# Performance work log

Measured on AMD Instinct MI355X. Metric: run time of the kernel, lower is better.

The kernel has to match this reference:

```python
import jax, jax.numpy as jnp
import numpy as np

B, N, M = 4, 50000, 256
BIN_MIN, BIN_MAX = -3.0, 3.0


def setup_inputs() -> dict:
    key = jax.random.key(0)
    kx, ky = jax.random.split(key)
    x_coords = jax.random.normal(kx, (B, N), dtype=jnp.float32)
    y_coords = jax.random.normal(ky, (B, N), dtype=jnp.float32)
    bins = jnp.linspace(BIN_MIN, BIN_MAX, M, dtype=jnp.float32)
    return {"x_coords": x_coords, "y_coords": y_coords, "bins": bins}


def reference(x_coords, y_coords, bins):
    # bandwidth defaults to bin resolution (bins[1] - bins[0])
    bandwidth = bins[1] - bins[0]
    # per-axis Gaussian kernel values: (B, N, M)
    kx = jnp.exp(-0.5 * jnp.square((x_coords[..., None] - bins) / bandwidth))
    ky = jnp.exp(-0.5 * jnp.square((y_coords[..., None] - bins) / bandwidth))
    # joint kernel values reduced over particles: (B, M, M)
    joint = jnp.einsum("bni,bnj->bij", kx, ky)
    norm = jnp.sum(joint, axis=(-2, -1), keepdims=True) + 1e-10
    return joint / norm
```

## Files before the change

### kernel.cpp

```cpp
#include <hip/hip_runtime.h>


#define B_     4
#define N_     50000
#define M_     256
#define NCH    32
#define NST    2
#define CHUNK  ((N_ + NCH - 1) / NCH)
#define BLOCK  1024
#define NWAVE  (BLOCK / 64)
#define GROWS  128
#define GCELLS (GROWS * M_)
#define GP64   16384
#define G64SZ  16576
#define CS2    0.72134752f
#define L127   6.9886847f

#if __has_builtin(__builtin_amdgcn_exp2f)
  #define EXP2(t) __builtin_amdgcn_exp2f(t)
#else
  #define EXP2(t) exp2f(t)
#endif

__device__ __forceinline__ unsigned short bf16ru(float f) {
    return (unsigned short)((__builtin_bit_cast(unsigned, f) + 0x8000u) >> 16);
}
__device__ __forceinline__ float bf2f(unsigned short u) {
    return __builtin_bit_cast(float, ((unsigned)u) << 16);
}

__global__ __launch_bounds__(BLOCK) void kde_accum(
    const float* __restrict__ xs, const float* __restrict__ ys,
    const float* __restrict__ bins, unsigned short* __restrict__ partial,
    float* __restrict__ ws2, int wide)
{
    __shared__ __align__(16) unsigned long long G64[G64SZ];
    __shared__ float sred[NWAVE];

    const int tid   = threadIdx.x;
    const int strip = blockIdx.x;
    const int chunk = blockIdx.y;
    const int b     = blockIdx.z;
    const int lane  = tid & 63;
    const int w     = tid >> 6;

    const float bin0  = bins[0];
    const float invbw = 1.0f / (bins[1] - bin0);
    const int   rlo   = strip * GROWS;

    {
        uint4* gz = (uint4*)G64;
        const uint4 z4 = {0u, 0u, 0u, 0u};
        for (int t = tid; t < G64SZ / 2; t += BLOCK) gz[t] = z4;
    }
    __syncthreads();

    const int start = chunk * CHUNK;
    const int end   = (start + CHUNK < N_) ? (start + CHUNK) : N_;
    const float* xp = xs + (size_t)b * N_;
    const float* yp = ys + (size_t)b * N_;

    const unsigned dmp = (unsigned)(GP64 + lane);

    int k = start + tid;
    float x = 3.0e30f, y = 3.0e30f;
    if (k < end) { x = xp[k]; y = yp[k]; }
    for (; k < end; k += BLOCK) {
        float xn = 3.0e30f, yn = 3.0e30f;
        if (k + BLOCK < end) { xn = xp[k + BLOCK]; yn = yp[k + BLOCK]; }

        const float ux  = (x - bin0) * invbw;
        const float uy  = (y - bin0) * invbw;
        const float stx = rintf(ux) - 3.0f;
        const float sty = rintf(uy) - 3.0f;
        const int rx = (int)stx;
        const int ry = (int)sty;

        if (rx + 6 >= rlo && rx < rlo + GROWS && ry + 6 >= 0 && ry < M_) {
            const float dx0 = ux - stx;
            const float dy0 = uy - sty;
            unsigned qx[7], qy[7];
            #pragma unroll
            for (int j = 0; j < 7; ++j) {
                const float dx = dx0 - (float)j;
                const float dy = dy0 - (float)j;
                qx[j] = (unsigned)(int)(EXP2(fmaf(-CS2 * dx, dx, L127)) + 0.5f);
                qy[j] = (unsigned)(int)(EXP2(fmaf(-CS2 * dy, dy, L127)) + 0.5f);
            }
            const int s  = ry & 1;
            const int pb0 = (ry - s) >> 1;
            const unsigned lo0 = s ? 0u    : qy[0], hi0 = s ? qy[0] : qy[1];
            const unsigned lo1 = s ? qy[1] : qy[2], hi1 = s ? qy[2] : qy[3];
            const unsigned lo2 = s ? qy[3] : qy[4], hi2 = s ? qy[4] : qy[5];
            const unsigned lo3 = s ? qy[5] : qy[6], hi3 = s ? qy[6] : 0u;
            unsigned long long ypk[4];
            ypk[0] = (unsigned long long)lo0 | ((unsigned long long)hi0 << 32);
            ypk[1] = (unsigned long long)lo1 | ((unsigned long long)hi1 << 32);
            ypk[2] = (unsigned long long)lo2 | ((unsigned long long)hi2 << 32);
            ypk[3] = (unsigned long long)lo3 | ((unsigned long long)hi3 << 32);
            unsigned pofs[4];
            #pragma unroll
            for (int t = 0; t < 4; ++t) {
                const int p = pb0 + t;
                pofs[t] = ((unsigned)p < 128u) ? (unsigned)p : 0x80000000u;
            }
            #pragma unroll
            for (int i = 0; i < 7; ++i) {
                const int rr = rx + i - rlo;
                const unsigned rbase =
                    ((unsigned)rr < (unsigned)GROWS) ? (unsigned)(rr << 7) : dmp;
                const unsigned long long wxi = (unsigned long long)qx[i];
                #pragma unroll
                for (int t = 0; t < 4; ++t) {
                    unsigned a = rbase + pofs[t];
                    a = ((int)a < 0) ? dmp : a;
                    atomicAdd(&G64[a], wxi * ypk[t]);
                }
            }
        }
        x = xn; y = yn;
    }
    __syncthreads();

    const unsigned int* Gv = (const unsigned int*)G64;
    unsigned short* pb = partial + (((size_t)chunk * B_ + b) << 16);
    float tsum = 0.f;
    #pragma unroll
    for (int rep = 0; rep < GCELLS / (BLOCK * 4); ++rep) {
        const int cell = rep * (BLOCK * 4) + tid * 4;
        const uint4 gv = *(const uint4*)&Gv[cell];
        const float f0 = (float)gv.x, f1 = (float)gv.y;
        const float f2 = (float)gv.z, f3 = (float)gv.w;
        tsum += (f0 + f1) + (f2 + f3);
        ushort4 o;
        o.x = bf16ru(f0); o.y = bf16ru(f1); o.z = bf16ru(f2); o.w = bf16ru(f3);
        const int r = cell >> 8;
        const int c = cell & (M_ - 1);
        *(ushort4*)&pb[(size_t)(rlo + r) * M_ + c] = o;
    }

    #pragma unroll
    for (int off = 32; off; off >>= 1) tsum += __shfl_xor(tsum, off);
    if (lane == 0) sred[w] = tsum;
    __syncthreads();
    if (tid == 0) {
        float bsum = 0.f;
        #pragma unroll
        for (int i = 0; i < NWAVE; ++i) bsum += sred[i];
        if (wide) {
            const int bid = (b * NCH + chunk) * NST + strip;
            ws2[bid] = bsum;
        } else {
            atomicAdd(&ws2[b], bsum);
        }
    }
}

__global__ __launch_bounds__(256) void kde_tail(
    const unsigned short* __restrict__ partial, const float* __restrict__ ws2,
    float* __restrict__ out, int wide)
{
    __shared__ float sred[4];
    __shared__ float snorm;
    const int tid = threadIdx.x;
    const int cellIdx = blockIdx.x * 256 + tid;
    const int bb = cellIdx >> 14;
    const int cb = cellIdx & 16383;

    float nrm;
    if (wide) {
        float t = (tid < NCH * NST) ? ws2[bb * (NCH * NST) + tid] : 0.f;
        #pragma unroll
        for (int off = 32; off; off >>= 1) t += __shfl_xor(t, off);
        if ((tid & 63) == 0) sred[tid >> 6] = t;
        __syncthreads();
        if (tid == 0) snorm = sred[0] + sred[1] + sred[2] + sred[3];
        __syncthreads();
        nrm = snorm;
    } else {
        nrm = ws2[bb];
    }

    float4 a = {0.f, 0.f, 0.f, 0.f};
    #pragma unroll 4
    for (int c = 0; c < NCH; ++c) {
        const ushort4 v = *(const ushort4*)(partial +
            (((size_t)c * B_ + bb) << 16) + (size_t)cb * 4);
        a.x += bf2f(v.x); a.y += bf2f(v.y); a.z += bf2f(v.z); a.w += bf2f(v.w);
    }
    const float sc = 1.0f / (nrm + 1e-10f);
    a.x *= sc; a.y *= sc; a.z *= sc; a.w *= sc;
    ((float4*)out)[cellIdx] = a;
}

extern "C" void kernel_launch(void* const* d_in, const int* in_sizes, int n_in,
                              void* d_out, int out_size, void* d_ws, size_t ws_size,
                              hipStream_t stream)
{
    const float* xs   = (const float*)d_in[0];
    const float* ys   = (const float*)d_in[1];
    const float* bins = (const float*)d_in[2];
    float* out = (float*)d_out;

    unsigned short* partial = (unsigned short*)d_ws;
    const size_t PSZ = (size_t)NCH * B_ * M_ * M_ * sizeof(unsigned short);
    float* ws2 = (float*)((char*)d_ws + PSZ);

    const int wide = (ws_size >= PSZ + 4096) ? 1 : 0;
    if (!wide) hipMemsetAsync(ws2, 0, 4 * sizeof(float), stream);

    kde_accum<<<dim3(NST, NCH, B_), dim3(BLOCK), 0, stream>>>(
        xs, ys, bins, partial, ws2, wide);
    kde_tail<<<dim3(B_ * M_ * M_ / (4 * 256)), dim3(256), 0, stream>>>(
        partial, ws2, out, wide);
}
```

Baseline: 75.11 us.

## Fuse accumulation and tail into one cooperative kernel with grid sync

Merges the accumulation kernel and the reduction/normalisation tail into a single cooperative launch, using a grid-wide barrier between the phases. After the barrier each block sums the per-block partial norms for its batch and reduces its slice of the bf16 partial grids into the output. The aim is to remove the second kernel launch and its gap. The cost is a grid barrier across 256 blocks of 1024 threads, which needs all of them co-resident. The new tail also does scalar rather than vectorised loads, and it drops the fallback path for a small workspace.

```diff
diff --git a/kernel.cpp b/kernel.cpp
--- a/kernel.cpp
+++ b/kernel.cpp
@@ -1,4 +1,5 @@
 #include <hip/hip_runtime.h>
+#include <hip/hip_cooperative_groups.h>
 
 
 #define B_     4
@@ -22,6 +23,8 @@
   #define EXP2(t) exp2f(t)
 #endif
 
+namespace cg = cooperative_groups;
+
 __device__ __forceinline__ unsigned short bf16ru(float f) {
     return (unsigned short)((__builtin_bit_cast(unsigned, f) + 0x8000u) >> 16);
 }
@@ -29,13 +32,14 @@
     return __builtin_bit_cast(float, ((unsigned)u) << 16);
 }
 
-__global__ __launch_bounds__(BLOCK) void kde_accum(
+__global__ __launch_bounds__(BLOCK) void kde_fused(
     const float* __restrict__ xs, const float* __restrict__ ys,
     const float* __restrict__ bins, unsigned short* __restrict__ partial,
-    float* __restrict__ ws2, int wide)
+    float* __restrict__ ws2, float* __restrict__ out)
 {
     __shared__ __align__(16) unsigned long long G64[G64SZ];
     __shared__ float sred[NWAVE];
+    __shared__ float snorm;
 
     const int tid   = threadIdx.x;
     const int strip = blockIdx.x;
@@ -147,50 +151,31 @@
         float bsum = 0.f;
         #pragma unroll
         for (int i = 0; i < NWAVE; ++i) bsum += sred[i];
-        if (wide) {
-            const int bid = (b * NCH + chunk) * NST + strip;
-            ws2[bid] = bsum;
-        } else {
-            atomicAdd(&ws2[b], bsum);
-        }
-    }
-}
-
-__global__ __launch_bounds__(256) void kde_tail(
-    const unsigned short* __restrict__ partial, const float* __restrict__ ws2,
-    float* __restrict__ out, int wide)
-{
-    __shared__ float sred[4];
-    __shared__ float snorm;
-    const int tid = threadIdx.x;
-    const int cellIdx = blockIdx.x * 256 + tid;
-    const int bb = cellIdx >> 14;
-    const int cb = cellIdx & 16383;
-
-    float nrm;
-    if (wide) {
-        float t = (tid < NCH * NST) ? ws2[bb * (NCH * NST) + tid] : 0.f;
-        #pragma unroll
-        for (int off = 32; off; off >>= 1) t += __shfl_xor(t, off);
-        if ((tid & 63) == 0) sred[tid >> 6] = t;
-        __syncthreads();
-        if (tid == 0) snorm = sred[0] + sred[1] + sred[2] + sred[3];
-        __syncthreads();
-        nrm = snorm;
-    } else {
-        nrm = ws2[bb];
+        ws2[(b * NCH + chunk) * NST + strip] = bsum;
     }
 
-    float4 a = {0.f, 0.f, 0.f, 0.f};
-    #pragma unroll 4
-    for (int c = 0; c < NCH; ++c) {
-        const ushort4 v = *(const ushort4*)(partial +
-            (((size_t)c * B_ + bb) << 16) + (size_t)cb * 4);
-        a.x += bf2f(v.x); a.y += bf2f(v.y); a.z += bf2f(v.z); a.w += bf2f(v.w);
+    cg::this_grid().sync();
+
+    {
+        float t = 0.f;
+        if (tid < NST * NCH) t = ws2[(b << 6) + tid];
+        if (w == 0) {
+            #pragma unroll
+            for (int off = 32; off; off >>= 1) t += __shfl_xor(t, off);
+            if (lane == 0) snorm = t;
+        }
+        __syncthreads();
     }
-    const float sc = 1.0f / (nrm + 1e-10f);
-    a.x *= sc; a.y *= sc; a.z *= sc; a.w *= sc;
-    ((float4*)out)[cellIdx] = a;
+    const float sc = 1.0f / (snorm + 1e-10f);
+
+    const int fid = (((b * NCH + chunk) * NST + strip) << 10) + tid;
+    const int bb = fid >> 16;
+    const int cb = fid & 65535;
+    float a = 0.f;
+    #pragma unroll
+    for (int c = 0; c < NCH; ++c)
+        a += bf2f(partial[(((size_t)c * B_ + bb) << 16) + cb]);
+    out[fid] = a * sc;
 }
 
 extern "C" void kernel_launch(void* const* d_in, const int* in_sizes, int n_in,
@@ -206,11 +191,9 @@
     const size_t PSZ = (size_t)NCH * B_ * M_ * M_ * sizeof(unsigned short);
     float* ws2 = (float*)((char*)d_ws + PSZ);
 
-    const int wide = (ws_size >= PSZ + 4096) ? 1 : 0;
-    if (!wide) hipMemsetAsync(ws2, 0, 4 * sizeof(float), stream);
-
-    kde_accum<<<dim3(NST, NCH, B_), dim3(BLOCK), 0, stream>>>(
-        xs, ys, bins, partial, ws2, wide);
-    kde_tail<<<dim3(B_ * M_ * M_ / (4 * 256)), dim3(256), 0, stream>>>(
-        partial, ws2, out, wide);
+    void* args[] = { (void*)&xs, (void*)&ys, (void*)&bins,
+                     (void*)&partial, (void*)&ws2, (void*)&out };
+    hipLaunchCooperativeKernel((const void*)kde_fused,
+                               dim3(NST, NCH, B_), dim3(BLOCK),
+                               args, 0, stream);
 }
```

After: 107.1 us. +42.5%, slower.

## Fuse final reduction into accumulate kernel via per-batch spin barrier

Applied to the files above, without the earlier changes.

Each accumulate block writes its partial sum, bumps a per-batch counter, and spins with a bounded timeout until all 64 blocks of its batch have arrived. It then reduces the bf16 partial histograms across chunks and writes normalized output directly, so the tail kernel's work and launch gap can be skipped. The tail kernel stays as a fallback and exits early when a batch's counter shows completion. This depends on all blocks being co-resident (256 blocks of 1024 threads with large LDS use), adds an extra memset, and any block that times out falls back to the tail path.

```diff
diff --git a/kernel.cpp b/kernel.cpp
--- a/kernel.cpp
+++ b/kernel.cpp
@@ -15,6 +15,7 @@
 #define G64SZ  16576
 #define CS2    0.72134752f
 #define L127   6.9886847f
+#define SPIN   100000
 
 #if __has_builtin(__builtin_amdgcn_exp2f)
   #define EXP2(t) __builtin_amdgcn_exp2f(t)
@@ -29,13 +30,16 @@
     return __builtin_bit_cast(float, ((unsigned)u) << 16);
 }
 
-__global__ __launch_bounds__(BLOCK) void kde_accum(
+
+__global__ __launch_bounds__(BLOCK) void kde_fused(
     const float* __restrict__ xs, const float* __restrict__ ys,
     const float* __restrict__ bins, unsigned short* __restrict__ partial,
-    float* __restrict__ ws2, int wide)
+    float* __restrict__ ws2, int* __restrict__ ctrl, float* __restrict__ out)
 {
     __shared__ __align__(16) unsigned long long G64[G64SZ];
     __shared__ float sred[NWAVE];
+    __shared__ float snorm;
+    __shared__ int   sok;
 
     const int tid   = threadIdx.x;
     const int strip = blockIdx.x;
@@ -147,18 +151,50 @@
         float bsum = 0.f;
         #pragma unroll
         for (int i = 0; i < NWAVE; ++i) bsum += sred[i];
-        if (wide) {
-            const int bid = (b * NCH + chunk) * NST + strip;
-            ws2[bid] = bsum;
-        } else {
-            atomicAdd(&ws2[b], bsum);
+        ws2[(b * NCH + chunk) * NST + strip] = bsum;
+    }
+    __syncthreads();
+
+    if (tid == 0) {
+        __threadfence();
+        atomicAdd(&ctrl[b * 32], 1);
+        int ok = 0;
+        for (int i = 0; i < SPIN; ++i) {
+            if (__hip_atomic_load(&ctrl[b * 32], __ATOMIC_RELAXED,
+                                  __HIP_MEMORY_SCOPE_AGENT) >= 64) { ok = 1; break; }
+            __builtin_amdgcn_s_sleep(4);
         }
-    }
+        sok = ok;
+    }
+    __syncthreads();
+    if (!sok) return;
+    __threadfence();
+
+    {
+        float t = (tid < NST * NCH) ? ws2[(b << 6) + tid] : 0.f;
+        if (w == 0) {
+            #pragma unroll
+            for (int off = 32; off; off >>= 1) t += __shfl_xor(t, off);
+            if (lane == 0) snorm = t;
+        }
+        __syncthreads();
+    }
+    const float sc = 1.0f / (snorm + 1e-10f);
+
+    const int fid = (((b * NCH + chunk) * NST + strip) << 10) + tid;
+    const int cb = fid & 65535;
+    float a = 0.f;
+    #pragma unroll
+    for (int c = 0; c < NCH; ++c)
+        a += bf2f(partial[(((size_t)c * B_ + b) << 16) + cb]);
+    out[fid] = a * sc;
+
+    if (tid == 0) atomicAdd(&ctrl[256 + b * 32], 1);
 }
 
 __global__ __launch_bounds__(256) void kde_tail(
     const unsigned short* __restrict__ partial, const float* __restrict__ ws2,
-    float* __restrict__ out, int wide)
+    const int* __restrict__ ctrl, float* __restrict__ out)
 {
     __shared__ float sred[4];
     __shared__ float snorm;
@@ -167,22 +203,19 @@
     const int bb = cellIdx >> 14;
     const int cb = cellIdx & 16383;
 
-    float nrm;
-    if (wide) {
-        float t = (tid < NCH * NST) ? ws2[bb * (NCH * NST) + tid] : 0.f;
-        #pragma unroll
-        for (int off = 32; off; off >>= 1) t += __shfl_xor(t, off);
-        if ((tid & 63) == 0) sred[tid >> 6] = t;
-        __syncthreads();
-        if (tid == 0) snorm = sred[0] + sred[1] + sred[2] + sred[3];
-        __syncthreads();
-        nrm = snorm;
-    } else {
-        nrm = ws2[bb];
-    }
+    if (ctrl[256 + bb * 32] == 64) return;
+
+    float t = (tid < NST * NCH) ? ws2[bb * (NST * NCH) + tid] : 0.f;
+    #pragma unroll
+    for (int off = 32; off; off >>= 1) t += __shfl_xor(t, off);
+    if ((tid & 63) == 0) sred[tid >> 6] = t;
+    __syncthreads();
+    if (tid == 0) snorm = sred[0] + sred[1] + sred[2] + sred[3];
+    __syncthreads();
+    const float nrm = snorm;
 
     float4 a = {0.f, 0.f, 0.f, 0.f};
-    #pragma unroll 4
+    #pragma unroll
     for (int c = 0; c < NCH; ++c) {
         const ushort4 v = *(const ushort4*)(partial +
             (((size_t)c * B_ + bb) << 16) + (size_t)cb * 4);
@@ -204,13 +237,12 @@
 
     unsigned short* partial = (unsigned short*)d_ws;
     const size_t PSZ = (size_t)NCH * B_ * M_ * M_ * sizeof(unsigned short);
-    float* ws2 = (float*)((char*)d_ws + PSZ);
-
-    const int wide = (ws_size >= PSZ + 4096) ? 1 : 0;
-    if (!wide) hipMemsetAsync(ws2, 0, 4 * sizeof(float), stream);
-
-    kde_accum<<<dim3(NST, NCH, B_), dim3(BLOCK), 0, stream>>>(
-        xs, ys, bins, partial, ws2, wide);
+    float* ws2  = (float*)((char*)d_ws + PSZ);
+    int*   ctrl = (int*)((char*)d_ws + PSZ + 4096);
+
+    hipMemsetAsync(ctrl, 0, 2048, stream);
+    kde_fused<<<dim3(NST, NCH, B_), dim3(BLOCK), 0, stream>>>(
+        xs, ys, bins, partial, ws2, ctrl, out);
     kde_tail<<<dim3(B_ * M_ * M_ / (4 * 256)), dim3(256), 0, stream>>>(
-        partial, ws2, out, wide);
-}
+        partial, ws2, ctrl, out);
+}
```

Result: slower. 138.9 us (+85.0%).
